# Optimization experiments

Measured on AMD Instinct MI355X. Metric: run time of the kernel, lower is better.

## Reference

```python
import jax, jax.numpy as jnp
import numpy as np

HIDDEN = 2048
QUANTILES = 16
BATCH = 8192
HALF = HIDDEN // 2


def setup_inputs() -> dict:
    key = jax.random.key(0)
    kx, k1, kb1, k2 = jax.random.split(key, 4)
    x = jax.random.normal(kx, (BATCH, HIDDEN), dtype=jnp.float32)
    # Stacked per-head params: head q computes Linear(H->H/2) -> GELU -> Linear(H/2->1)
    # PyTorch Linear default init ~ U(-1/sqrt(fan_in), 1/sqrt(fan_in)); last layer kaiming-normal, bias 0.
    lim1 = 1.0 / np.sqrt(HIDDEN)
    W1 = jax.random.uniform(k1, (QUANTILES, HIDDEN, HALF), minval=-lim1, maxval=lim1, dtype=jnp.float32)
    b1 = jax.random.uniform(kb1, (QUANTILES, HALF), minval=-lim1, maxval=lim1, dtype=jnp.float32)
    # kaiming_normal fan_in, linear nonlinearity -> std = 1/sqrt(fan_in)
    W2 = jax.random.normal(k2, (QUANTILES, HALF), dtype=jnp.float32) / np.sqrt(HALF)
    b2 = jnp.zeros((QUANTILES,), dtype=jnp.float32)
    return {"x": x, "W1": W1, "b1": b1, "W2": W2, "b2": b2}


def reference(x, W1, b1, W2, b2):
    # Batched over all quantile heads: one grouped GEMM + fused GELU + grouped GEMV.
    # h: [batch, quantiles, half]
    h = jnp.einsum('bh,qhk->bqk', x, W1) + b1[None, :, :]
    h = jax.nn.gelu(h, approximate=False)  # torch nn.GELU() default = exact erf GELU
    # out: [batch, quantiles]
    out = jnp.einsum('bqk,qk->bq', h, W2) + b2[None, :]
    return out
```

## Files before the change

kernel.cpp:

```cpp
#include <hip/hip_runtime.h>

#define HIDDEN 2048
#define QUANT  16
#define BATCH  8192
#define HALFD  1024

#define BM 256
#define BN 256
#define BKT 32
#define NT (HIDDEN / BKT)
#define NT2 (NT / 2)
#define A_HALFS (BM * BKT)
#define SLOT_HALFS (2 * A_HALFS)

typedef _Float16 half8  __attribute__((ext_vector_type(8)));
typedef float    floatx16 __attribute__((ext_vector_type(16)));

__device__ __forceinline__ void load_lds16(const void* gptr, void* lptr) {
  __builtin_amdgcn_global_load_lds(
      (const __attribute__((address_space(1))) void*)gptr,
      (__attribute__((address_space(3))) void*)lptr, 16, 0, 0);
}

__device__ __forceinline__ float gelu_exact(float v) {
  const float z  = 0.7071067811865476f * v;
  const float az = fabsf(z);
  const float t  = __builtin_amdgcn_rcpf(1.0f + 0.3275911f * az);
  const float p  = t * (0.254829592f +
                   t * (-0.284496736f +
                   t * (1.421413741f +
                   t * (-1.453152027f +
                   t * 1.061405429f))));
  float er = 1.0f - p * __expf(-az * az);
  er = copysignf(er, z);
  return 0.5f * v * (1.0f + er);
}

__global__ __launch_bounds__(256) void convert_x_kernel(const float* __restrict__ x,
                                                        _Float16* __restrict__ xh) {
  const int i = (blockIdx.x * 256 + threadIdx.x) * 8;
  const float4 a = *(const float4*)(x + i);
  const float4 b = *(const float4*)(x + i + 4);
  half8 h;
  h[0] = (_Float16)a.x; h[1] = (_Float16)a.y; h[2] = (_Float16)a.z; h[3] = (_Float16)a.w;
  h[4] = (_Float16)b.x; h[5] = (_Float16)b.y; h[6] = (_Float16)b.z; h[7] = (_Float16)b.w;
  *(half8*)(xh + i) = h;
}

__global__ __launch_bounds__(256) void transpose_w1_kernel(const float* __restrict__ W1,
                                                           _Float16* __restrict__ W1T) {
  __shared__ float tile[64][33];
  const int q  = blockIdx.z;
  const int h0 = blockIdx.y * 64;
  const int n0 = blockIdx.x * 32;
  const float* src = W1 + (size_t)q * HIDDEN * HALFD;
  _Float16*    dst = W1T + (size_t)q * HALFD * HIDDEN;
  const int t  = threadIdx.x;
  const int lr = t >> 3;
  const int lc = (t & 7) * 4;
  #pragma unroll
  for (int j = 0; j < 2; ++j) {
    const float4 v = *(const float4*)(src + (size_t)(h0 + lr + 32 * j) * HALFD + n0 + lc);
    tile[lr + 32 * j][lc + 0] = v.x;
    tile[lr + 32 * j][lc + 1] = v.y;
    tile[lr + 32 * j][lc + 2] = v.z;
    tile[lr + 32 * j][lc + 3] = v.w;
  }
  __syncthreads();
  const int sn = t >> 3;
  const int sh = (t & 7) * 8;
  half8 v;
  #pragma unroll
  for (int c = 0; c < 8; ++c) v[c] = (_Float16)tile[sh + c][sn];
  *(half8*)(dst + (size_t)(n0 + sn) * HIDDEN + h0 + sh) = v;
}

__global__ __launch_bounds__(256) void init_out_kernel(float* __restrict__ out,
                                                       const float* __restrict__ b2) {
  const int i = blockIdx.x * 256 + threadIdx.x;
  out[i] = b2[i & (QUANT - 1)];
}

__global__ __launch_bounds__(512, 2) void qhead_gemm_kernel(
    const _Float16* __restrict__ A,
    const _Float16* __restrict__ BT,
    const float* __restrict__ b1,
    const float* __restrict__ W2,
    float* __restrict__ out) {
  extern __shared__ _Float16 lds[];

  const int tid  = threadIdx.x;
  const int lane = tid & 63;
  const int wave = tid >> 6;
  const int wm = wave >> 2, wn = wave & 3;
  const int r31 = lane & 31, l5 = lane >> 5;
  const int fsw = (r31 >> 1) & 3;

  const int flat = blockIdx.x;
  const int wg = (flat & 7) * 256 + (flat >> 3);
  const int mb = wg >> 6;
  const int qn = wg & 63;
  const int q  = qn >> 2;
  const int nb = qn & 3;
  const int m0 = mb << 8;

  const _Float16* Ablk = A + (size_t)m0 * HIDDEN;
  const _Float16* Bblk = BT + ((size_t)q * HALFD + nb * BN) * HIDDEN;

  const int srow = tid >> 2;
  const int skg  = (tid & 3) ^ ((srow >> 1) & 3);
  const _Float16* agp = Ablk + (size_t)srow * HIDDEN + skg * 8;
  const _Float16* bgp = Bblk + (size_t)srow * HIDDEN + skg * 8;

  int aoff[4], boff[2];
  #pragma unroll
  for (int mf = 0; mf < 4; ++mf) aoff[mf] = (wm * 128 + mf * 32 + r31) * BKT;
  #pragma unroll
  for (int nf = 0; nf < 2; ++nf) boff[nf] = (wn * 64 + nf * 32 + r31) * BKT + A_HALFS;

  floatx16 acc[4][2];
  #pragma unroll
  for (int mf = 0; mf < 4; ++mf)
    #pragma unroll
    for (int nf = 0; nf < 2; ++nf)
      #pragma unroll
      for (int i = 0; i < 16; ++i) acc[mf][nf][i] = 0.f;

#define STAGE_A(ts_) do {                                                  \
    const int ts_a = (ts_);                                                \
    const int kc_a = ((ts_a < NT) ? ts_a : (ts_a - NT)) * BKT;             \
    _Float16* ld_a = lds + (ts_a & 3) * SLOT_HALFS + tid * 8;              \
    load_lds16(agp + kc_a, ld_a);                                          \
    load_lds16(agp + kc_a + (size_t)128 * HIDDEN, ld_a + 4096);            \
  } while (0)

#define STAGE_B(ts_) do {                                                  \
    const int ts_b = (ts_);                                                \
    const int kc_b = ((ts_b < NT) ? ts_b : (ts_b - NT)) * BKT;             \
    _Float16* ld_b = lds + (ts_b & 3) * SLOT_HALFS + A_HALFS + tid * 8;    \
    load_lds16(bgp + kc_b, ld_b);                                          \
    load_lds16(bgp + kc_b + (size_t)128 * HIDDEN, ld_b + 4096);            \
  } while (0)

#define PHASE(LS, KS, STAGE_STMT, DO_VM) do {                              \
    const _Float16* ls_ = (LS);                                            \
    const int p_ = (((KS << 1) | l5) ^ fsw) << 3;                          \
    half8 af0 = *(const half8*)(ls_ + aoff[0] + p_);                       \
    half8 af1 = *(const half8*)(ls_ + aoff[1] + p_);                       \
    half8 af2 = *(const half8*)(ls_ + aoff[2] + p_);                       \
    half8 af3 = *(const half8*)(ls_ + aoff[3] + p_);                       \
    half8 bf0 = *(const half8*)(ls_ + boff[0] + p_);                       \
    half8 bf1 = *(const half8*)(ls_ + boff[1] + p_);                       \
    STAGE_STMT;                                                            \
    asm volatile("s_barrier" ::: "memory");                                \
    asm volatile("s_waitcnt lgkmcnt(0)" ::: "memory");                     \
    __builtin_amdgcn_sched_barrier(0);                                     \
    __builtin_amdgcn_s_setprio(1);                                         \
    acc[0][0] = __builtin_amdgcn_mfma_f32_32x32x16_f16(af0, bf0, acc[0][0], 0, 0, 0); \
    acc[0][1] = __builtin_amdgcn_mfma_f32_32x32x16_f16(af0, bf1, acc[0][1], 0, 0, 0); \
    acc[1][0] = __builtin_amdgcn_mfma_f32_32x32x16_f16(af1, bf0, acc[1][0], 0, 0, 0); \
    acc[1][1] = __builtin_amdgcn_mfma_f32_32x32x16_f16(af1, bf1, acc[1][1], 0, 0, 0); \
    acc[2][0] = __builtin_amdgcn_mfma_f32_32x32x16_f16(af2, bf0, acc[2][0], 0, 0, 0); \
    acc[2][1] = __builtin_amdgcn_mfma_f32_32x32x16_f16(af2, bf1, acc[2][1], 0, 0, 0); \
    acc[3][0] = __builtin_amdgcn_mfma_f32_32x32x16_f16(af3, bf0, acc[3][0], 0, 0, 0); \
    acc[3][1] = __builtin_amdgcn_mfma_f32_32x32x16_f16(af3, bf1, acc[3][1], 0, 0, 0); \
    __builtin_amdgcn_s_setprio(0);                                         \
    __builtin_amdgcn_sched_barrier(0);                                     \
    if (DO_VM) asm volatile("s_waitcnt vmcnt(8)" ::: "memory");            \
    asm volatile("s_barrier" ::: "memory");                                \
  } while (0)

  STAGE_A(0); STAGE_B(0); STAGE_A(1); STAGE_B(1); STAGE_A(2); STAGE_B(2);
  asm volatile("s_waitcnt vmcnt(8)\n\ts_barrier" ::: "memory");

  #pragma unroll 2
  for (int t = 0; t < NT2; ++t) {
    const _Float16* ls0 = lds + ((2 * t) & 3) * SLOT_HALFS;
    const _Float16* ls1 = lds + ((2 * t + 1) & 3) * SLOT_HALFS;
    PHASE(ls0, 0, STAGE_A(2 * t + 3), 0);
    PHASE(ls0, 1, STAGE_B(2 * t + 3), 1);
    PHASE(ls1, 0, STAGE_A(2 * t + 4), 0);
    PHASE(ls1, 1, STAGE_B(2 * t + 4), 1);
  }
#undef PHASE
#undef STAGE_A
#undef STAGE_B

  const int colb = nb * BN + wn * 64;
  #pragma unroll
  for (int mf = 0; mf < 4; ++mf) {
    float rs[16];
    #pragma unroll
    for (int r = 0; r < 16; ++r) rs[r] = 0.f;
    #pragma unroll
    for (int nf = 0; nf < 2; ++nf) {
      const int ncol = colb + nf * 32 + r31;
      const float b1v = b1[q * HALFD + ncol];
      const float w2v = W2[q * HALFD + ncol];
      #pragma unroll
      for (int r = 0; r < 16; ++r)
        rs[r] += gelu_exact(acc[mf][nf][r] + b1v) * w2v;
    }
    #pragma unroll
    for (int r = 0; r < 16; ++r) {
      float v = rs[r];
      v += __shfl_xor(v, 1, 64);
      v += __shfl_xor(v, 2, 64);
      v += __shfl_xor(v, 4, 64);
      v += __shfl_xor(v, 8, 64);
      v += __shfl_xor(v, 16, 64);
      rs[r] = v;
    }
    if (r31 == 0) {
      const int mbase = m0 + wm * 128 + mf * 32 + 4 * l5;
      #pragma unroll
      for (int r = 0; r < 16; ++r) {
        const int mrow = mbase + (r & 3) + 8 * (r >> 2);
        atomicAdd(&out[(size_t)mrow * QUANT + q], rs[r]);
      }
    }
  }
}

extern "C" void kernel_launch(void* const* d_in, const int* in_sizes, int n_in,
                              void* d_out, int out_size, void* d_ws, size_t ws_size,
                              hipStream_t stream) {
  const float* x  = (const float*)d_in[0];
  const float* W1 = (const float*)d_in[1];
  const float* b1 = (const float*)d_in[2];
  const float* W2 = (const float*)d_in[3];
  const float* b2 = (const float*)d_in[4];
  float* out = (float*)d_out;

  _Float16* xh  = (_Float16*)d_ws;
  _Float16* w1t = (_Float16*)((char*)d_ws +
                  (size_t)BATCH * HIDDEN * sizeof(_Float16));

  static int lds_cfg = 0;
  if (!lds_cfg) {
    hipFuncSetAttribute(reinterpret_cast<const void*>(qhead_gemm_kernel),
                        hipFuncAttributeMaxDynamicSharedMemorySize, 131072);
    lds_cfg = 1;
  }

  convert_x_kernel<<<BATCH * HIDDEN / (256 * 8), 256, 0, stream>>>(x, xh);
  transpose_w1_kernel<<<dim3(HALFD / 32, HIDDEN / 64, QUANT), 256, 0, stream>>>(W1, w1t);
  init_out_kernel<<<BATCH * QUANT / 256, 256, 0, stream>>>(out, b2);
  qhead_gemm_kernel<<<dim3(BATCH / BM * (QUANT * HALFD / BN)), 512, 131072, stream>>>(
      xh, w1t, b1, W2, out);
}
```

Before: 881.0 us.

## Double-buffer MFMA operand registers to prefetch next LDS fragments during compute

Adds two register buffer sets so each phase issues the LDS reads for the next k-substep's A/B fragments before running MFMAs on the current set. The wait changes from lgkmcnt(0) to lgkmcnt(6), and the extra barrier before compute is removed. The vmcnt waits are moved to different phases. The aim is to hide LDS read latency behind the matrix instructions, at the cost of more VGPRs and a more delicate hazard ordering between the global-to-LDS loads and the LDS reads.

```diff
diff --git a/kernel.cpp b/kernel.cpp
--- a/kernel.cpp
+++ b/kernel.cpp
@@ -126,6 +126,8 @@
       #pragma unroll
       for (int i = 0; i < 16; ++i) acc[mf][nf][i] = 0.f;
 
+  half8 r0[6], r1[6];
+
 #define STAGE_A(ts_) do {                                                  \
     const int ts_a = (ts_);                                                \
     const int kc_a = ((ts_a < NT) ? ts_a : (ts_a - NT)) * BKT;             \
@@ -142,45 +144,55 @@
     load_lds16(bgp + kc_b + (size_t)128 * HIDDEN, ld_b + 4096);            \
   } while (0)
 
-#define PHASE(LS, KS, STAGE_STMT, DO_VM) do {                              \
-    const _Float16* ls_ = (LS);                                            \
-    const int p_ = (((KS << 1) | l5) ^ fsw) << 3;                          \
-    half8 af0 = *(const half8*)(ls_ + aoff[0] + p_);                       \
-    half8 af1 = *(const half8*)(ls_ + aoff[1] + p_);                       \
-    half8 af2 = *(const half8*)(ls_ + aoff[2] + p_);                       \
-    half8 af3 = *(const half8*)(ls_ + aoff[3] + p_);                       \
-    half8 bf0 = *(const half8*)(ls_ + boff[0] + p_);                       \
-    half8 bf1 = *(const half8*)(ls_ + boff[1] + p_);                       \
+#define PHASE(CUR, NXT, LSN, KSN, STAGE_STMT, DO_VM4) do {                 \
+    const _Float16* lsn_ = (LSN);                                          \
+    const int pn_ = ((((KSN) << 1) | l5) ^ fsw) << 3;                      \
+    NXT[0] = *(const half8*)(lsn_ + aoff[0] + pn_);                        \
+    NXT[1] = *(const half8*)(lsn_ + aoff[1] + pn_);                        \
+    NXT[2] = *(const half8*)(lsn_ + aoff[2] + pn_);                        \
+    NXT[3] = *(const half8*)(lsn_ + aoff[3] + pn_);                        \
+    NXT[4] = *(const half8*)(lsn_ + boff[0] + pn_);                        \
+    NXT[5] = *(const half8*)(lsn_ + boff[1] + pn_);                        \
     STAGE_STMT;                                                            \
-    asm volatile("s_barrier" ::: "memory");                                \
-    asm volatile("s_waitcnt lgkmcnt(0)" ::: "memory");                     \
+    asm volatile("s_waitcnt lgkmcnt(6)" ::: "memory");                     \
     __builtin_amdgcn_sched_barrier(0);                                     \
     __builtin_amdgcn_s_setprio(1);                                         \
-    acc[0][0] = __builtin_amdgcn_mfma_f32_32x32x16_f16(af0, bf0, acc[0][0], 0, 0, 0); \
-    acc[0][1] = __builtin_amdgcn_mfma_f32_32x32x16_f16(af0, bf1, acc[0][1], 0, 0, 0); \
-    acc[1][0] = __builtin_amdgcn_mfma_f32_32x32x16_f16(af1, bf0, acc[1][0], 0, 0, 0); \
-    acc[1][1] = __builtin_amdgcn_mfma_f32_32x32x16_f16(af1, bf1, acc[1][1], 0, 0, 0); \
-    acc[2][0] = __builtin_amdgcn_mfma_f32_32x32x16_f16(af2, bf0, acc[2][0], 0, 0, 0); \
-    acc[2][1] = __builtin_amdgcn_mfma_f32_32x32x16_f16(af2, bf1, acc[2][1], 0, 0, 0); \
-    acc[3][0] = __builtin_amdgcn_mfma_f32_32x32x16_f16(af3, bf0, acc[3][0], 0, 0, 0); \
-    acc[3][1] = __builtin_amdgcn_mfma_f32_32x32x16_f16(af3, bf1, acc[3][1], 0, 0, 0); \
+    acc[0][0] = __builtin_amdgcn_mfma_f32_32x32x16_f16(CUR[0], CUR[4], acc[0][0], 0, 0, 0); \
+    acc[0][1] = __builtin_amdgcn_mfma_f32_32x32x16_f16(CUR[0], CUR[5], acc[0][1], 0, 0, 0); \
+    acc[1][0] = __builtin_amdgcn_mfma_f32_32x32x16_f16(CUR[1], CUR[4], acc[1][0], 0, 0, 0); \
+    acc[1][1] = __builtin_amdgcn_mfma_f32_32x32x16_f16(CUR[1], CUR[5], acc[1][1], 0, 0, 0); \
+    acc[2][0] = __builtin_amdgcn_mfma_f32_32x32x16_f16(CUR[2], CUR[4], acc[2][0], 0, 0, 0); \
+    acc[2][1] = __builtin_amdgcn_mfma_f32_32x32x16_f16(CUR[2], CUR[5], acc[2][1], 0, 0, 0); \
+    acc[3][0] = __builtin_amdgcn_mfma_f32_32x32x16_f16(CUR[3], CUR[4], acc[3][0], 0, 0, 0); \
+    acc[3][1] = __builtin_amdgcn_mfma_f32_32x32x16_f16(CUR[3], CUR[5], acc[3][1], 0, 0, 0); \
     __builtin_amdgcn_s_setprio(0);                                         \
     __builtin_amdgcn_sched_barrier(0);                                     \
-    if (DO_VM) asm volatile("s_waitcnt vmcnt(8)" ::: "memory");            \
+    if (DO_VM4) asm volatile("s_waitcnt vmcnt(4)" ::: "memory");           \
     asm volatile("s_barrier" ::: "memory");                                \
   } while (0)
 
   STAGE_A(0); STAGE_B(0); STAGE_A(1); STAGE_B(1); STAGE_A(2); STAGE_B(2);
   asm volatile("s_waitcnt vmcnt(8)\n\ts_barrier" ::: "memory");
+
+  {
+    const int p0 = (l5 ^ fsw) << 3;
+    r0[0] = *(const half8*)(lds + aoff[0] + p0);
+    r0[1] = *(const half8*)(lds + aoff[1] + p0);
+    r0[2] = *(const half8*)(lds + aoff[2] + p0);
+    r0[3] = *(const half8*)(lds + aoff[3] + p0);
+    r0[4] = *(const half8*)(lds + boff[0] + p0);
+    r0[5] = *(const half8*)(lds + boff[1] + p0);
+  }
 
   #pragma unroll 2
   for (int t = 0; t < NT2; ++t) {
     const _Float16* ls0 = lds + ((2 * t) & 3) * SLOT_HALFS;
     const _Float16* ls1 = lds + ((2 * t + 1) & 3) * SLOT_HALFS;
-    PHASE(ls0, 0, STAGE_A(2 * t + 3), 0);
-    PHASE(ls0, 1, STAGE_B(2 * t + 3), 1);
-    PHASE(ls1, 0, STAGE_A(2 * t + 4), 0);
-    PHASE(ls1, 1, STAGE_B(2 * t + 4), 1);
+    const _Float16* ls2 = lds + ((2 * t + 2) & 3) * SLOT_HALFS;
+    PHASE(r0, r1, ls0, 1, STAGE_A(2 * t + 3), 1);
+    PHASE(r1, r0, ls1, 0, STAGE_B(2 * t + 3), 0);
+    PHASE(r0, r1, ls1, 1, STAGE_A(2 * t + 4), 1);
+    PHASE(r1, r0, ls2, 0, STAGE_B(2 * t + 4), 0);
   }
 #undef PHASE
 #undef STAGE_A
```

Result: no change. 877.2 us (-0.4%).
